# Optimization experiments

Measured on AMD Instinct MI355X. Metric: run time of the kernel, lower is better.

Reference implementation:

```python
import jax, jax.numpy as jnp
import numpy as np
from jax.scipy.linalg import expm

B, T, DIM = 8, 4096, 256


def setup_inputs() -> dict:
    key = jax.random.key(0)
    k1, k2 = jax.random.split(key)
    psi = jax.random.normal(k1, (B, T, 4, DIM), dtype=jnp.float32)
    H = jax.random.normal(k2, (4, DIM, DIM), dtype=jnp.float32) * 0.02
    return {"psi": psi, "H": H}


def reference(psi, H):
    # H_complex = H[0] + i*H[1]; components H[2], H[3] are unused (as in the torch code)
    H_complex = (H[0] + 1j * H[1]).astype(jnp.complex64)
    # Unitary-like evolution operator U = expm(-i * H_complex), [dim, dim] complex64
    U = expm(-1j * H_complex)
    # All 4 quaternion components share the same U -> one batched complex matmul
    psi_c = psi.astype(jnp.complex64)  # [B, T, 4, dim]
    evolved = jnp.einsum('btcd,de->btce', psi_c, U)  # complex matmul over last dim
    # Torch code keeps only the real part of each evolved component
    return evolved.real.astype(jnp.float32)
```

## Files before the change

kernel.cpp:

```cpp
#include <hip/hip_runtime.h>

#define NDIM 256
#define NN (NDIM*NDIM)

typedef __attribute__((ext_vector_type(8))) short s8bf;
typedef __attribute__((ext_vector_type(4))) float f32x4;

__device__ __forceinline__ unsigned short f2bf(float f) {
    union { float f; unsigned u; } v; v.f = f;
    unsigned u = v.u;
    return (unsigned short)((u + 0x7FFFu + ((u >> 16) & 1u)) >> 16);
}

__global__ __launch_bounds__(1024) void kmm(
    const float* __restrict__ H, float2* __restrict__ M2c, float2* __restrict__ M3c,
    unsigned short* __restrict__ Ut, int mode) {
    __shared__ float2 As[16][257];
    __shared__ float2 Bs[256][17];
    __shared__ float2 Rs[3][16][17];
    const int tx = threadIdx.x, ty = threadIdx.y, tz = threadIdx.z;
    const int tid = (tz * 16 + ty) * 16 + tx;
    const int r0 = blockIdx.y * 16, c0 = blockIdx.x * 16;

#pragma unroll
    for (int i = 0; i < 4; ++i) {
        int idx = i * 1024 + tid;
        int r = idx >> 8, k = idx & 255;
        float2 a;
        if (mode == 0)      { a.x = H[NN + (r0+r)*NDIM + k]; a.y = -H[(r0+r)*NDIM + k]; }
        else if (mode == 1) a = M2c[(r0+r)*NDIM + k];
        else                a = M3c[(r0+r)*NDIM + k];
        As[r][k] = a;
    }
#pragma unroll
    for (int i = 0; i < 4; ++i) {
        int idx = i * 1024 + tid;
        int k = idx >> 4, cc = idx & 15;
        float2 b;
        if (mode <= 1) { b.x = H[NN + k*NDIM + c0+cc]; b.y = -H[k*NDIM + c0+cc]; }
        else {
            int g = k * NDIM + c0 + cc;
            float mr = H[NN + g], mi = -H[g];
            float2 m2 = M2c[g], m3 = M3c[g];
            float di = (k == c0 + cc) ? 1.f : 0.f;
            b.x = di*(1.f/6.f) + mr*(1.f/24.f) + m2.x*(1.f/120.f) + m3.x*(1.f/720.f);
            b.y =                mi*(1.f/24.f) + m2.y*(1.f/120.f) + m3.y*(1.f/720.f);
        }
        Bs[k][cc] = b;
    }
    __syncthreads();

    float sr0=0.f, si0=0.f, sr1=0.f, si1=0.f;
#pragma unroll 8
    for (int k = tz*64; k < tz*64 + 64; k += 2) {
        float2 a = As[ty][k], b = Bs[k][tx];
        sr0 = fmaf(a.x, b.x, sr0); sr0 = fmaf(-a.y, b.y, sr0);
        si0 = fmaf(a.x, b.y, si0); si0 = fmaf(a.y, b.x, si0);
        float2 a1 = As[ty][k+1], b1 = Bs[k+1][tx];
        sr1 = fmaf(a1.x, b1.x, sr1); sr1 = fmaf(-a1.y, b1.y, sr1);
        si1 = fmaf(a1.x, b1.y, si1); si1 = fmaf(a1.y, b1.x, si1);
    }
    float sr = sr0 + sr1, si = si0 + si1;
    if (tz > 0) Rs[tz-1][ty][tx] = make_float2(sr, si);
    __syncthreads();
    if (tz == 0) {
        sr += Rs[0][ty][tx].x + Rs[1][ty][tx].x + Rs[2][ty][tx].x;
        si += Rs[0][ty][tx].y + Rs[1][ty][tx].y + Rs[2][ty][tx].y;
        int d = r0 + ty, e = c0 + tx;
        if (mode == 0)      M2c[d*NDIM + e] = make_float2(sr, si);
        else if (mode == 1) M3c[d*NDIM + e] = make_float2(sr, si);
        else {
            int g = d * NDIM + e;
            float ur = sr + ((d == e) ? 1.f : 0.f) + H[NN + g] + M2c[g].x * 0.5f;
            Ut[e * NDIM + d] = f2bf(ur);
        }
    }
}

__global__ __launch_bounds__(512, 1) void kgemm(
    const float* __restrict__ psi, const unsigned short* __restrict__ Ut,
    float* __restrict__ out) {
    __shared__ unsigned short Bls[NN];
    __shared__ float Escr[8][512];
    const int t = threadIdx.x;

    const s8bf* Ug = (const s8bf*)Ut;
    s8bf* Bg = (s8bf*)Bls;
#pragma unroll
    for (int i = 0; i < 16; ++i) {
        int g = i * 512 + t;
        int r = g >> 5, j = g & 31;
        Bg[(r << 5) | (j ^ (r & 7))] = Ug[g];
    }
    __syncthreads();

    const int w = t >> 6, lane = t & 63;
    const int c = lane & 15, q = lane >> 4;
    const f32x4* psi4 = (const f32x4*)psi;
    f32x4* out4 = (f32x4*)out;
    float* Ebase = &Escr[w][0];

#pragma unroll 1
    for (int st = 0; st < 2; ++st) {
        const int base = blockIdx.x * 512 + w * 64 + st * 32;
        const size_t rl = (size_t)(base + c) * 64;
        const size_t rh = rl + (size_t)16 * 64;

        f32x4 acc[32];
#pragma unroll
        for (int i = 0; i < 32; ++i) acc[i] = (f32x4)0.f;

        f32x4 pl0 = psi4[rl + q*2], pl1 = psi4[rl + q*2 + 1];
        f32x4 ph0 = psi4[rh + q*2], ph1 = psi4[rh + q*2 + 1];

#pragma unroll
        for (int s = 0; s < 8; ++s) {
            f32x4 nl0, nl1, nh0, nh1;
            if (s < 7) {
                int o = (s + 1) * 8 + q * 2;
                nl0 = psi4[rl + o]; nl1 = psi4[rl + o + 1];
                nh0 = psi4[rh + o]; nh1 = psi4[rh + o + 1];
            } else { nl0 = pl0; nl1 = pl1; nh0 = ph0; nh1 = ph1; }
            s8bf alo, ahi;
#pragma unroll
            for (int j = 0; j < 4; ++j) {
                alo[j]   = (short)f2bf(pl0[j]); alo[j+4] = (short)f2bf(pl1[j]);
                ahi[j]   = (short)f2bf(ph0[j]); ahi[j+4] = (short)f2bf(ph1[j]);
            }
#pragma unroll
            for (int ct = 0; ct < 16; ++ct) {
                int rr = ct * 16 + c;
                s8bf bb = Bg[(rr << 5) | ((s*4 + q) ^ (rr & 7))];
                acc[ct]      = __builtin_amdgcn_mfma_f32_16x16x32_bf16(alo, bb, acc[ct],      0, 0, 0);
                acc[16 + ct] = __builtin_amdgcn_mfma_f32_16x16x32_bf16(ahi, bb, acc[16 + ct], 0, 0, 0);
            }
            pl0 = nl0; pl1 = nl1; ph0 = nh0; ph1 = nh1;
        }

#pragma unroll
        for (int p = 0; p < 32; ++p) {
            const int half = p >> 4, qq = (p >> 2) & 3, rr = p & 3;
            float* E = Ebase + (p & 1) * 256;
            if (q == qq) {
#pragma unroll
                for (int ct = 0; ct < 16; ++ct)
                    E[ct * 16 + c] = acc[half * 16 + ct][rr];
            }
            f32x4 vv = *(const f32x4*)(&E[lane * 4]);
            __builtin_nontemporal_store(vv,
                &out4[(size_t)(base + half * 16 + qq * 4 + rr) * 64 + lane]);
            __builtin_amdgcn_sched_barrier(0);
        }
    }
}

extern "C" void kernel_launch(void* const* d_in, const int* in_sizes, int n_in,
                              void* d_out, int out_size, void* d_ws, size_t ws_size,
                              hipStream_t stream) {
    const float* psi = (const float*)d_in[0];
    const float* H   = (const float*)d_in[1];
    float* out = (float*)d_out;

    float2* M2c = (float2*)d_ws;
    float2* M3c = M2c + NN;
    unsigned short* Ut = (unsigned short*)(M3c + NN);

    dim3 cb(16, 16, 4), cg(16, 16);
    kmm<<<cg, cb, 0, stream>>>(H, M2c, M3c, Ut, 0);
    kmm<<<cg, cb, 0, stream>>>(H, M2c, M3c, Ut, 1);
    kmm<<<cg, cb, 0, stream>>>(H, M2c, M3c, Ut, 2);
    kgemm<<<256, 512, 0, stream>>>(psi, Ut, out);
}
```

Baseline: 74.02 us.

## Use 1024-thread GEMM blocks with 16-row tiles per wave and double-buffered psi loads

The GEMM kernel moves from 512 to 1024 threads per block. Each wave now handles one 16-row tile per step instead of two, which halves the accumulator registers, and psi loads are double-buffered two k-steps ahead. Float-to-bf16 conversion now uses the HIP intrinsic instead of manual rounding. More waves are meant to hide memory latency, at the cost of fewer MFMAs per B-fragment LDS read and a larger LDS scratch area.

```diff
diff --git a/kernel.cpp b/kernel.cpp
--- a/kernel.cpp
+++ b/kernel.cpp
@@ -1,4 +1,5 @@
 #include <hip/hip_runtime.h>
+#include <hip/hip_bf16.h>
 
 #define NDIM 256
 #define NN (NDIM*NDIM)
@@ -10,6 +11,11 @@
     union { float f; unsigned u; } v; v.f = f;
     unsigned u = v.u;
     return (unsigned short)((u + 0x7FFFu + ((u >> 16) & 1u)) >> 16);
+}
+__device__ __forceinline__ short f2bfs(float f) {
+    __hip_bfloat16 h = __float2bfloat16(f);
+    union { __hip_bfloat16 h; short s; } v; v.h = h;
+    return v.s;
 }
 
 __global__ __launch_bounds__(1024) void kmm(
@@ -77,18 +83,18 @@
     }
 }
 
-__global__ __launch_bounds__(512, 1) void kgemm(
+__global__ __launch_bounds__(1024, 4) void kgemm(
     const float* __restrict__ psi, const unsigned short* __restrict__ Ut,
     float* __restrict__ out) {
     __shared__ unsigned short Bls[NN];
-    __shared__ float Escr[8][512];
+    __shared__ float Escr[16][512];
     const int t = threadIdx.x;
 
     const s8bf* Ug = (const s8bf*)Ut;
     s8bf* Bg = (s8bf*)Bls;
 #pragma unroll
-    for (int i = 0; i < 16; ++i) {
-        int g = i * 512 + t;
+    for (int i = 0; i < 8; ++i) {
+        int g = i * 1024 + t;
         int r = g >> 5, j = g & 31;
         Bg[(r << 5) | (j ^ (r & 7))] = Ug[g];
     }
@@ -102,53 +108,49 @@
 
 #pragma unroll 1
     for (int st = 0; st < 2; ++st) {
-        const int base = blockIdx.x * 512 + w * 64 + st * 32;
+        const int base = blockIdx.x * 512 + st * 256 + w * 16;
         const size_t rl = (size_t)(base + c) * 64;
-        const size_t rh = rl + (size_t)16 * 64;
 
-        f32x4 acc[32];
+        f32x4 acc[16];
 #pragma unroll
-        for (int i = 0; i < 32; ++i) acc[i] = (f32x4)0.f;
+        for (int i = 0; i < 16; ++i) acc[i] = (f32x4)0.f;
 
-        f32x4 pl0 = psi4[rl + q*2], pl1 = psi4[rl + q*2 + 1];
-        f32x4 ph0 = psi4[rh + q*2], ph1 = psi4[rh + q*2 + 1];
+        f32x4 pb[2][2];
+        pb[0][0] = psi4[rl + q*2];     pb[0][1] = psi4[rl + q*2 + 1];
+        pb[1][0] = psi4[rl + 8 + q*2]; pb[1][1] = psi4[rl + 8 + q*2 + 1];
 
 #pragma unroll
         for (int s = 0; s < 8; ++s) {
-            f32x4 nl0, nl1, nh0, nh1;
-            if (s < 7) {
-                int o = (s + 1) * 8 + q * 2;
-                nl0 = psi4[rl + o]; nl1 = psi4[rl + o + 1];
-                nh0 = psi4[rh + o]; nh1 = psi4[rh + o + 1];
-            } else { nl0 = pl0; nl1 = pl1; nh0 = ph0; nh1 = ph1; }
-            s8bf alo, ahi;
+            s8bf a;
 #pragma unroll
             for (int j = 0; j < 4; ++j) {
-                alo[j]   = (short)f2bf(pl0[j]); alo[j+4] = (short)f2bf(pl1[j]);
-                ahi[j]   = (short)f2bf(ph0[j]); ahi[j+4] = (short)f2bf(ph1[j]);
+                a[j]     = f2bfs(pb[s & 1][0][j]);
+                a[j + 4] = f2bfs(pb[s & 1][1][j]);
+            }
+            if (s < 6) {
+                int o = (s + 2) * 8 + q * 2;
+                pb[s & 1][0] = psi4[rl + o];
+                pb[s & 1][1] = psi4[rl + o + 1];
             }
 #pragma unroll
             for (int ct = 0; ct < 16; ++ct) {
                 int rr = ct * 16 + c;
                 s8bf bb = Bg[(rr << 5) | ((s*4 + q) ^ (rr & 7))];
-                acc[ct]      = __builtin_amdgcn_mfma_f32_16x16x32_bf16(alo, bb, acc[ct],      0, 0, 0);
-                acc[16 + ct] = __builtin_amdgcn_mfma_f32_16x16x32_bf16(ahi, bb, acc[16 + ct], 0, 0, 0);
+                acc[ct] = __builtin_amdgcn_mfma_f32_16x16x32_bf16(a, bb, acc[ct], 0, 0, 0);
             }
-            pl0 = nl0; pl1 = nl1; ph0 = nh0; ph1 = nh1;
         }
 
 #pragma unroll
-        for (int p = 0; p < 32; ++p) {
-            const int half = p >> 4, qq = (p >> 2) & 3, rr = p & 3;
+        for (int p = 0; p < 16; ++p) {
+            const int qq = p >> 2, rr = p & 3;
             float* E = Ebase + (p & 1) * 256;
             if (q == qq) {
 #pragma unroll
                 for (int ct = 0; ct < 16; ++ct)
-                    E[ct * 16 + c] = acc[half * 16 + ct][rr];
+                    E[ct * 16 + c] = acc[ct][rr];
             }
             f32x4 vv = *(const f32x4*)(&E[lane * 4]);
-            __builtin_nontemporal_store(vv,
-                &out4[(size_t)(base + half * 16 + qq * 4 + rr) * 64 + lane]);
+            __builtin_nontemporal_store(vv, &out4[(size_t)(base + p) * 64 + lane]);
             __builtin_amdgcn_sched_barrier(0);
         }
     }
@@ -169,5 +171,5 @@
     kmm<<<cg, cb, 0, stream>>>(H, M2c, M3c, Ut, 0);
     kmm<<<cg, cb, 0, stream>>>(H, M2c, M3c, Ut, 1);
     kmm<<<cg, cb, 0, stream>>>(H, M2c, M3c, Ut, 2);
-    kgemm<<<256, 512, 0, stream>>>(psi, Ut, out);
+    kgemm<<<256, 1024, 0, stream>>>(psi, Ut, out);
 }
```

Result: faster. 72.21 us, median of 3 (-2.4%).
